# Performance work log

Measured on AMD Instinct MI355X. Metric: run time of the kernel, lower is better.

The kernel has to match this reference:

```python
import jax, jax.numpy as jnp
import numpy as np

EPS = 1e-6

def setup_inputs() -> dict:
    key = jax.random.key(0)
    kq, kk, kv = jax.random.split(key, 3)
    n, L, h, d = 4, 8192, 8, 64
    queries = jax.random.normal(kq, (n, L, h, d), dtype=jnp.float32)
    keys = jax.random.normal(kk, (n, L, h, d), dtype=jnp.float32)
    values = jax.random.normal(kv, (n, L, h, d), dtype=jnp.float32)
    return {"queries": queries, "keys": keys, "values": values}

def reference(queries, keys, values):
    d = queries.shape[-1]
    temp = d ** (-0.25)  # softmax_temp default e**-0.25
    # elu feature map: phi(x) = elu(x) + 1  (applied after temperature scaling)
    q = jax.nn.elu(queries * temp) + 1.0  # [n, l, h, d]
    k = jax.nn.elu(keys * temp) + 1.0     # [n, s, h, d]
    # associative kv state: [n, h, m, d]
    kv = jnp.einsum('nshd,nshm->nhmd', k, values)
    # normalizer z: [n, l, h]
    z = 1.0 / (jnp.einsum('nlhd,nhd->nlh', q, k.sum(axis=1)) + EPS)
    # output: [n, l, h, m]
    v = jnp.einsum('nlhd,nhmd,nlh->nlhm', q, kv, z)
    # module returns v.transpose(-3, -2) -> [n, h, l, m]
    return jnp.swapaxes(v, 1, 2)
```

## Files before the change

### kernel.cpp

```cpp
#include <hip/hip_runtime.h>
#include <hip/hip_bf16.h>

#define NN 4
#define LL 8192
#define HH 8
#define DD 64
#define NH 32
#define RS  (HH*DD)
#define KV_ELEMS 4160
#define CCH 32

typedef __attribute__((ext_vector_type(8))) short bf16x8;
typedef __attribute__((ext_vector_type(4))) float f32x4;

__device__ __forceinline__ float phi(float x) {
  float t = x * 0.35355339059327373f;
  return t > 0.f ? t + 1.f : __expf(t);
}
__device__ __forceinline__ short f2bf(float x) {
  __hip_bfloat16 h = __float2bfloat16(x);
  return (short)__builtin_bit_cast(unsigned short, h);
}
__device__ __forceinline__ float bf2f(short s) {
  __hip_bfloat16 h = __builtin_bit_cast(__hip_bfloat16, (unsigned short)s);
  return __bfloat162float(h);
}
__device__ __forceinline__ void split2(float x, short& hi, short& lo) {
  hi = f2bf(x);
  lo = f2bf(x - bf2f(hi));
}

__global__ __launch_bounds__(256) void kv_partial_kernel(
    const float* __restrict__ K, const float* __restrict__ V,
    float* __restrict__ part, int sch)
{
  const int nh    = blockIdx.x / sch;
  const int chunk = blockIdx.x % sch;
  const int n = nh >> 3, h = nh & 7;
  const int tid = threadIdx.x;
  const int w = tid >> 6, lane = tid & 63;
  const int q = lane >> 4, p = lane & 15;
  const int d_super = (w >> 1) * 32, m_super = (w & 1) * 32;
  const int rows_pb = LL / sch;
  const int s_base  = chunk * rows_pb;

  const float* kbase = K + ((size_t)n * LL * HH + h) * DD;
  const float* vbase = V + ((size_t)n * LL * HH + h) * DD;

  f32x4 acc[2][2] = {};
  float ksacc[2] = {0.f, 0.f};

  for (int step = 0; step < rows_pb / 32; ++step) {
    const int s0 = s_base + step * 32 + q * 8;

    bf16x8 ahi[2], alo[2];
#pragma unroll
    for (int dt = 0; dt < 2; ++dt) {
      const float* kp = kbase + (size_t)s0 * RS + d_super + dt * 16 + p;
      float f[8];
#pragma unroll
      for (int j = 0; j < 8; ++j) f[j] = phi(kp[(size_t)j * RS]);
#pragma unroll
      for (int j = 0; j < 8; ++j) ksacc[dt] += f[j];
#pragma unroll
      for (int j = 0; j < 8; ++j) { short hi, lo; split2(f[j], hi, lo); ahi[dt][j] = hi; alo[dt][j] = lo; }
    }

    bf16x8 bhi[2], blo[2];
#pragma unroll
    for (int mt = 0; mt < 2; ++mt) {
      const float* vp = vbase + (size_t)s0 * RS + m_super + mt * 16 + p;
      float f[8];
#pragma unroll
      for (int j = 0; j < 8; ++j) f[j] = vp[(size_t)j * RS];
#pragma unroll
      for (int j = 0; j < 8; ++j) { short hi, lo; split2(f[j], hi, lo); bhi[mt][j] = hi; blo[mt][j] = lo; }
    }

#pragma unroll
    for (int dt = 0; dt < 2; ++dt)
#pragma unroll
      for (int mt = 0; mt < 2; ++mt) {
        acc[dt][mt] = __builtin_amdgcn_mfma_f32_16x16x32_bf16(ahi[dt], bhi[mt], acc[dt][mt], 0, 0, 0);
        acc[dt][mt] = __builtin_amdgcn_mfma_f32_16x16x32_bf16(ahi[dt], blo[mt], acc[dt][mt], 0, 0, 0);
        acc[dt][mt] = __builtin_amdgcn_mfma_f32_16x16x32_bf16(alo[dt], bhi[mt], acc[dt][mt], 0, 0, 0);
      }
  }

#pragma unroll
  for (int dt = 0; dt < 2; ++dt) {
    ksacc[dt] += __shfl_xor(ksacc[dt], 16, 64);
    ksacc[dt] += __shfl_xor(ksacc[dt], 32, 64);
  }

  float* po = part + (size_t)blockIdx.x * KV_ELEMS;
#pragma unroll
  for (int dt = 0; dt < 2; ++dt)
#pragma unroll
    for (int mt = 0; mt < 2; ++mt) {
      const int row = d_super + dt * 16 + q * 4;
      const int col = m_super + mt * 16 + p;
#pragma unroll
      for (int r = 0; r < 4; ++r)
        po[(row + r) * 64 + col] = acc[dt][mt][r];
    }
  if ((w & 1) == 0 && q < 2)
    po[4096 + d_super + q * 16 + p] = ksacc[q];
}

__global__ __launch_bounds__(256) void kv_reduce_kernel(
    const float* __restrict__ part, short* __restrict__ kvh,
    short* __restrict__ kvl, float* __restrict__ ksum, int np)
{
  const int nh = blockIdx.x / 17;
  const int e  = (blockIdx.x % 17) * 256 + threadIdx.x;
  if (e >= KV_ELEMS) return;
  const float* pp = part + (size_t)nh * np * KV_ELEMS + e;
  float s = 0.f;
  for (int i = 0; i < np; ++i) s += pp[(size_t)i * KV_ELEMS];
  if (e < 4096) {
    const int d = e >> 6, m = e & 63;
    short hi, lo; split2(s, hi, lo);
    kvh[(size_t)nh * 4096 + m * 64 + d] = hi;
    kvl[(size_t)nh * 4096 + m * 64 + d] = lo;
  } else {
    ksum[(size_t)nh * 64 + (e - 4096)] = s;
  }
}

__global__ __launch_bounds__(256) void attn_out_kernel(
    const float* __restrict__ Q, const short* __restrict__ kvh,
    const short* __restrict__ kvl, const float* __restrict__ ksumg,
    float* __restrict__ out)
{
  const int nh    = blockIdx.x / CCH;
  const int chunk = blockIdx.x % CCH;
  const int n = nh >> 3, h = nh & 7;
  const int tid = threadIdx.x;
  const int w = tid >> 6, lane = tid & 63;
  const int q = lane >> 4, p = lane & 15;
  const int m_super = (w & 1) * 32;
  const int rows_pb = LL / CCH;
  const int row_base = chunk * rows_pb + (w >> 1) * (rows_pb / 2);

  const float* qbase = Q + ((size_t)n * LL * HH + h) * DD;

  bf16x8 bh[2][2], bl[2][2];
#pragma unroll
  for (int mt = 0; mt < 2; ++mt)
#pragma unroll
    for (int kst = 0; kst < 2; ++kst) {
      const size_t off = (size_t)nh * 4096 + (m_super + mt * 16 + p) * 64 + kst * 32 + q * 8;
      bh[mt][kst] = *(const bf16x8*)(kvh + off);
      bl[mt][kst] = *(const bf16x8*)(kvl + off);
    }
  float ksr[2][8];
#pragma unroll
  for (int kst = 0; kst < 2; ++kst) {
    const float* kp = ksumg + (size_t)nh * 64 + kst * 32 + q * 8;
    float4 a = *(const float4*)(kp), b = *(const float4*)(kp + 4);
    ksr[kst][0]=a.x; ksr[kst][1]=a.y; ksr[kst][2]=a.z; ksr[kst][3]=a.w;
    ksr[kst][4]=b.x; ksr[kst][5]=b.y; ksr[kst][6]=b.z; ksr[kst][7]=b.w;
  }

  for (int lt = 0; lt < rows_pb / 2 / 16; ++lt) {
    const int l0 = row_base + lt * 16;
    f32x4 acc[2] = {};
    float zpart = 0.f;

#pragma unroll
    for (int kst = 0; kst < 2; ++kst) {
      const float* qp = qbase + (size_t)(l0 + p) * RS + kst * 32 + q * 8;
      float4 f0 = *(const float4*)(qp), f1 = *(const float4*)(qp + 4);
      float f[8] = {f0.x, f0.y, f0.z, f0.w, f1.x, f1.y, f1.z, f1.w};
      bf16x8 ah, al;
#pragma unroll
      for (int j = 0; j < 8; ++j) {
        f[j] = phi(f[j]);
        short hi, lo; split2(f[j], hi, lo);
        ah[j] = hi; al[j] = lo;
        zpart += f[j] * ksr[kst][j];
      }
#pragma unroll
      for (int mt = 0; mt < 2; ++mt) {
        acc[mt] = __builtin_amdgcn_mfma_f32_16x16x32_bf16(ah, bh[mt][kst], acc[mt], 0, 0, 0);
        acc[mt] = __builtin_amdgcn_mfma_f32_16x16x32_bf16(ah, bl[mt][kst], acc[mt], 0, 0, 0);
        acc[mt] = __builtin_amdgcn_mfma_f32_16x16x32_bf16(al, bh[mt][kst], acc[mt], 0, 0, 0);
      }
    }

    zpart += __shfl_xor(zpart, 16, 64);
    zpart += __shfl_xor(zpart, 32, 64);
    const float z = 1.0f / (zpart + 1e-6f);
    float zr[4];
#pragma unroll
    for (int r = 0; r < 4; ++r) zr[r] = __shfl(z, q * 4 + r, 64);

#pragma unroll
    for (int mt = 0; mt < 2; ++mt) {
      const int col = m_super + mt * 16 + p;
#pragma unroll
      for (int r = 0; r < 4; ++r) {
        const int row = l0 + q * 4 + r;
        out[((size_t)nh * LL + row) * DD + col] = acc[mt][r] * zr[r];
      }
    }
  }
}

extern "C" void kernel_launch(void* const* d_in, const int* in_sizes, int n_in,
                              void* d_out, int out_size, void* d_ws, size_t ws_size,
                              hipStream_t stream)
{
  const float* Q = (const float*)d_in[0];
  const float* K = (const float*)d_in[1];
  const float* V = (const float*)d_in[2];
  float* out = (float*)d_out;

  int sch = 32;
  while (sch > 1) {
    size_t need = (size_t)NH * sch * KV_ELEMS * 4
                + (size_t)NH * 4096 * 2 * 2
                + (size_t)NH * 64 * 4;
    if (need <= ws_size) break;
    sch >>= 1;
  }
  float* part = (float*)d_ws;
  short* kvh  = (short*)((char*)d_ws + (size_t)NH * sch * KV_ELEMS * 4);
  short* kvl  = kvh + (size_t)NH * 4096;
  float* ksum = (float*)(kvl + (size_t)NH * 4096);

  hipLaunchKernelGGL(kv_partial_kernel, dim3(NH * sch), dim3(256), 0, stream,
                     K, V, part, sch);
  hipLaunchKernelGGL(kv_reduce_kernel, dim3(NH * 17), dim3(256), 0, stream,
                     part, kvh, kvl, ksum, sch);
  hipLaunchKernelGGL(attn_out_kernel, dim3(NH * CCH), dim3(256), 0, stream,
                     Q, kvh, kvl, ksum, out);
}
```

Baseline: 253.4 us.

## Stage K/V tiles through LDS with vectorized loads and register prefetch

Reworks the KV-partial kernel. Each thread now issues coalesced float4 loads of K and V rows and computes phi and the bf16 hi/lo split once per element. The split values are written transposed into LDS, and MFMA operands are read back from LDS. Before, the kernel did strided scalar global loads, and the four warps redundantly applied phi and split to overlapping K/V data. The next tile is prefetched into registers while MFMAs run, and the k-sum is reduced through LDS. This adds barriers and LDS traffic, and launch bounds now request 4 blocks per CU.

```diff
diff --git a/kernel.cpp b/kernel.cpp
--- a/kernel.cpp
+++ b/kernel.cpp
@@ -29,8 +29,12 @@
   hi = f2bf(x);
   lo = f2bf(x - bf2f(hi));
 }
-
-__global__ __launch_bounds__(256) void kv_partial_kernel(
+__device__ __forceinline__ int pk2(short a, short b) {
+  return (int)(((unsigned)(unsigned short)a) | (((unsigned)(unsigned short)b) << 16));
+}
+#define MFMA16 __builtin_amdgcn_mfma_f32_16x16x32_bf16
+
+__global__ __launch_bounds__(256, 4) void kv_partial_kernel(
     const float* __restrict__ K, const float* __restrict__ V,
     float* __restrict__ part, int sch)
 {
@@ -40,72 +44,102 @@
   const int tid = threadIdx.x;
   const int w = tid >> 6, lane = tid & 63;
   const int q = lane >> 4, p = lane & 15;
-  const int d_super = (w >> 1) * 32, m_super = (w & 1) * 32;
+  const int dsup = (w >> 1) * 32, msup = (w & 1) * 32;
+  const int g = tid >> 4, c = tid & 15;
   const int rows_pb = LL / sch;
+  const int ntiles  = rows_pb / 64;
   const int s_base  = chunk * rows_pb;
 
   const float* kbase = K + ((size_t)n * LL * HH + h) * DD;
   const float* vbase = V + ((size_t)n * LL * HH + h) * DD;
 
+  __shared__ __align__(16) short lds4[4][64][72];
+
   f32x4 acc[2][2] = {};
-  float ksacc[2] = {0.f, 0.f};
-
-  for (int step = 0; step < rows_pb / 32; ++step) {
-    const int s0 = s_base + step * 32 + q * 8;
-
-    bf16x8 ahi[2], alo[2];
-#pragma unroll
-    for (int dt = 0; dt < 2; ++dt) {
-      const float* kp = kbase + (size_t)s0 * RS + d_super + dt * 16 + p;
-      float f[8];
-#pragma unroll
-      for (int j = 0; j < 8; ++j) f[j] = phi(kp[(size_t)j * RS]);
-#pragma unroll
-      for (int j = 0; j < 8; ++j) ksacc[dt] += f[j];
-#pragma unroll
-      for (int j = 0; j < 8; ++j) { short hi, lo; split2(f[j], hi, lo); ahi[dt][j] = hi; alo[dt][j] = lo; }
-    }
-
-    bf16x8 bhi[2], blo[2];
+  float ksp[4] = {0.f, 0.f, 0.f, 0.f};
+  f32x4 kf[4], vf[4];
+
+#define LOADT(T) { \
+    const float* kp_ = kbase + (size_t)(s_base + (T) * 64 + 4 * g) * RS + 4 * c; \
+    const float* vp_ = vbase + (size_t)(s_base + (T) * 64 + 4 * g) * RS + 4 * c; \
+    kf[0] = *(const f32x4*)(kp_);          vf[0] = *(const f32x4*)(vp_); \
+    kf[1] = *(const f32x4*)(kp_ + RS);     vf[1] = *(const f32x4*)(vp_ + RS); \
+    kf[2] = *(const f32x4*)(kp_ + 2*RS);   vf[2] = *(const f32x4*)(vp_ + 2*RS); \
+    kf[3] = *(const f32x4*)(kp_ + 3*RS);   vf[3] = *(const f32x4*)(vp_ + 3*RS); }
+
+  LOADT(0);
+
+  for (int tile = 0; tile < ntiles; ++tile) {
+#pragma unroll
+    for (int j = 0; j < 4; ++j) {
+      short sh[4], sl[4];
+#pragma unroll
+      for (int u = 0; u < 4; ++u) {
+        float f = phi(kf[u][j]);
+        ksp[j] += f;
+        split2(f, sh[u], sl[u]);
+      }
+      *(int2*)&lds4[0][4*c + j][4*g] = make_int2(pk2(sh[0], sh[1]), pk2(sh[2], sh[3]));
+      *(int2*)&lds4[1][4*c + j][4*g] = make_int2(pk2(sl[0], sl[1]), pk2(sl[2], sl[3]));
+#pragma unroll
+      for (int u = 0; u < 4; ++u) split2(vf[u][j], sh[u], sl[u]);
+      *(int2*)&lds4[2][4*c + j][4*g] = make_int2(pk2(sh[0], sh[1]), pk2(sh[2], sh[3]));
+      *(int2*)&lds4[3][4*c + j][4*g] = make_int2(pk2(sl[0], sl[1]), pk2(sl[2], sl[3]));
+    }
+    __syncthreads();
+
+    if (tile + 1 < ntiles) LOADT(tile + 1);
+
+#pragma unroll
+    for (int ks = 0; ks < 2; ++ks) {
+      const int so = ks * 32 + q * 8;
+      bf16x8 ah[2], al[2], bh[2], bl[2];
+#pragma unroll
+      for (int dt = 0; dt < 2; ++dt) {
+        ah[dt] = *(const bf16x8*)&lds4[0][dsup + dt * 16 + p][so];
+        al[dt] = *(const bf16x8*)&lds4[1][dsup + dt * 16 + p][so];
+      }
+#pragma unroll
+      for (int mt = 0; mt < 2; ++mt) {
+        bh[mt] = *(const bf16x8*)&lds4[2][msup + mt * 16 + p][so];
+        bl[mt] = *(const bf16x8*)&lds4[3][msup + mt * 16 + p][so];
+      }
+#pragma unroll
+      for (int dt = 0; dt < 2; ++dt)
+#pragma unroll
+        for (int mt = 0; mt < 2; ++mt) {
+          acc[dt][mt] = MFMA16(ah[dt], bh[mt], acc[dt][mt], 0, 0, 0);
+          acc[dt][mt] = MFMA16(ah[dt], bl[mt], acc[dt][mt], 0, 0, 0);
+          acc[dt][mt] = MFMA16(al[dt], bh[mt], acc[dt][mt], 0, 0, 0);
+        }
+    }
+    __syncthreads();
+  }
+#undef LOADT
+
+  float* po = part + (size_t)blockIdx.x * KV_ELEMS;
+#pragma unroll
+  for (int dt = 0; dt < 2; ++dt)
 #pragma unroll
     for (int mt = 0; mt < 2; ++mt) {
-      const float* vp = vbase + (size_t)s0 * RS + m_super + mt * 16 + p;
-      float f[8];
-#pragma unroll
-      for (int j = 0; j < 8; ++j) f[j] = vp[(size_t)j * RS];
-#pragma unroll
-      for (int j = 0; j < 8; ++j) { short hi, lo; split2(f[j], hi, lo); bhi[mt][j] = hi; blo[mt][j] = lo; }
-    }
-
-#pragma unroll
-    for (int dt = 0; dt < 2; ++dt)
-#pragma unroll
-      for (int mt = 0; mt < 2; ++mt) {
-        acc[dt][mt] = __builtin_amdgcn_mfma_f32_16x16x32_bf16(ahi[dt], bhi[mt], acc[dt][mt], 0, 0, 0);
-        acc[dt][mt] = __builtin_amdgcn_mfma_f32_16x16x32_bf16(ahi[dt], blo[mt], acc[dt][mt], 0, 0, 0);
-        acc[dt][mt] = __builtin_amdgcn_mfma_f32_16x16x32_bf16(alo[dt], bhi[mt], acc[dt][mt], 0, 0, 0);
-      }
-  }
-
-#pragma unroll
-  for (int dt = 0; dt < 2; ++dt) {
-    ksacc[dt] += __shfl_xor(ksacc[dt], 16, 64);
-    ksacc[dt] += __shfl_xor(ksacc[dt], 32, 64);
-  }
-
-  float* po = part + (size_t)blockIdx.x * KV_ELEMS;
-#pragma unroll
-  for (int dt = 0; dt < 2; ++dt)
-#pragma unroll
-    for (int mt = 0; mt < 2; ++mt) {
-      const int row = d_super + dt * 16 + q * 4;
-      const int col = m_super + mt * 16 + p;
+      const int row = dsup + dt * 16 + q * 4;
+      const int col = msup + mt * 16 + p;
 #pragma unroll
       for (int r = 0; r < 4; ++r)
         po[(row + r) * 64 + col] = acc[dt][mt][r];
     }
-  if ((w & 1) == 0 && q < 2)
-    po[4096 + d_super + q * 16 + p] = ksacc[q];
+
+  float* ksl = (float*)lds4;
+  f32x4 kq = {ksp[0], ksp[1], ksp[2], ksp[3]};
+  *(f32x4*)&ksl[tid * 4] = kq;
+  __syncthreads();
+  if (tid < 64) {
+    float s = 0.f;
+#pragma unroll
+    for (int gg = 0; gg < 16; ++gg)
+      s += ksl[(gg * 16 + (tid >> 2)) * 4 + (tid & 3)];
+    po[4096 + tid] = s;
+  }
 }
 
 __global__ __launch_bounds__(256) void kv_reduce_kernel(
@@ -183,9 +217,9 @@
       }
 #pragma unroll
       for (int mt = 0; mt < 2; ++mt) {
-        acc[mt] = __builtin_amdgcn_mfma_f32_16x16x32_bf16(ah, bh[mt][kst], acc[mt], 0, 0, 0);
-        acc[mt] = __builtin_amdgcn_mfma_f32_16x16x32_bf16(ah, bl[mt][kst], acc[mt], 0, 0, 0);
-        acc[mt] = __builtin_amdgcn_mfma_f32_16x16x32_bf16(al, bh[mt][kst], acc[mt], 0, 0, 0);
+        acc[mt] = MFMA16(ah, bh[mt][kst], acc[mt], 0, 0, 0);
+        acc[mt] = MFMA16(ah, bl[mt][kst], acc[mt], 0, 0, 0);
+        acc[mt] = MFMA16(al, bh[mt][kst], acc[mt], 0, 0, 0);
       }
     }
 
```

Measured after the change: 258.2 us. About the same (+1.9%).

## Restructure KV and output kernels to load all heads per row coalesced via LDS

Applied to the files above, without the earlier changes.

Both main kernels now assign one block per batch and row chunk, with 512 threads covering all 8 heads. Each block loads full contiguous rows of K/V/Q with vectorized reads, stages them in shared memory and prefetches the next tile into registers. This replaces the previous strided per-head gathers, which touched only 64 floats of each 512-float row. The KV partial product switches from bf16-split MFMA to FP32 FMA register tiles. The output kernel now has each wave handle one head with all 64 output columns. The partial-buffer layout and the reduce indexing change to match. In exchange there are more LDS barriers, heavier register use per thread, and scalar FMA in place of matrix-core throughput for the KV product.

```diff
diff --git a/kernel.cpp b/kernel.cpp
--- a/kernel.cpp
+++ b/kernel.cpp
@@ -8,7 +8,7 @@
 #define NH 32
 #define RS  (HH*DD)
 #define KV_ELEMS 4160
-#define CCH 32
+#define CCH 64
 
 typedef __attribute__((ext_vector_type(8))) short bf16x8;
 typedef __attribute__((ext_vector_type(4))) float f32x4;
@@ -29,83 +29,95 @@
   hi = f2bf(x);
   lo = f2bf(x - bf2f(hi));
 }
-
-__global__ __launch_bounds__(256) void kv_partial_kernel(
+#define MFMA16 __builtin_amdgcn_mfma_f32_16x16x32_bf16
+
+__global__ __launch_bounds__(512, 2) void kv_partial_kernel(
     const float* __restrict__ K, const float* __restrict__ V,
     float* __restrict__ part, int sch)
 {
-  const int nh    = blockIdx.x / sch;
-  const int chunk = blockIdx.x % sch;
-  const int n = nh >> 3, h = nh & 7;
+  const int n = blockIdx.x / sch, chunk = blockIdx.x % sch;
   const int tid = threadIdx.x;
-  const int w = tid >> 6, lane = tid & 63;
-  const int q = lane >> 4, p = lane & 15;
-  const int d_super = (w >> 1) * 32, m_super = (w & 1) * 32;
+  const int h  = tid >> 6;
+  const int t6 = tid & 63;
+  const int d0 = ((t6 >> 3) & 7) * 8;
+  const int m0 = (t6 & 7) * 8;
+  const int hc = h * 64;
+  const int sr = tid >> 6, sc = (tid & 63) * 8;
   const int rows_pb = LL / sch;
-  const int s_base  = chunk * rows_pb;
-
-  const float* kbase = K + ((size_t)n * LL * HH + h) * DD;
-  const float* vbase = V + ((size_t)n * LL * HH + h) * DD;
-
-  f32x4 acc[2][2] = {};
-  float ksacc[2] = {0.f, 0.f};
-
-  for (int step = 0; step < rows_pb / 32; ++step) {
-    const int s0 = s_base + step * 32 + q * 8;
-
-    bf16x8 ahi[2], alo[2];
-#pragma unroll
-    for (int dt = 0; dt < 2; ++dt) {
-      const float* kp = kbase + (size_t)s0 * RS + d_super + dt * 16 + p;
-      float f[8];
-#pragma unroll
-      for (int j = 0; j < 8; ++j) f[j] = phi(kp[(size_t)j * RS]);
-#pragma unroll
-      for (int j = 0; j < 8; ++j) ksacc[dt] += f[j];
-#pragma unroll
-      for (int j = 0; j < 8; ++j) { short hi, lo; split2(f[j], hi, lo); ahi[dt][j] = hi; alo[dt][j] = lo; }
-    }
-
-    bf16x8 bhi[2], blo[2];
-#pragma unroll
-    for (int mt = 0; mt < 2; ++mt) {
-      const float* vp = vbase + (size_t)s0 * RS + m_super + mt * 16 + p;
-      float f[8];
-#pragma unroll
-      for (int j = 0; j < 8; ++j) f[j] = vp[(size_t)j * RS];
-#pragma unroll
-      for (int j = 0; j < 8; ++j) { short hi, lo; split2(f[j], hi, lo); bhi[mt][j] = hi; blo[mt][j] = lo; }
-    }
-
-#pragma unroll
-    for (int dt = 0; dt < 2; ++dt)
-#pragma unroll
-      for (int mt = 0; mt < 2; ++mt) {
-        acc[dt][mt] = __builtin_amdgcn_mfma_f32_16x16x32_bf16(ahi[dt], bhi[mt], acc[dt][mt], 0, 0, 0);
-        acc[dt][mt] = __builtin_amdgcn_mfma_f32_16x16x32_bf16(ahi[dt], blo[mt], acc[dt][mt], 0, 0, 0);
-        acc[dt][mt] = __builtin_amdgcn_mfma_f32_16x16x32_bf16(alo[dt], bhi[mt], acc[dt][mt], 0, 0, 0);
-      }
-  }
-
-#pragma unroll
-  for (int dt = 0; dt < 2; ++dt) {
-    ksacc[dt] += __shfl_xor(ksacc[dt], 16, 64);
-    ksacc[dt] += __shfl_xor(ksacc[dt], 32, 64);
-  }
-
-  float* po = part + (size_t)blockIdx.x * KV_ELEMS;
-#pragma unroll
-  for (int dt = 0; dt < 2; ++dt)
-#pragma unroll
-    for (int mt = 0; mt < 2; ++mt) {
-      const int row = d_super + dt * 16 + q * 4;
-      const int col = m_super + mt * 16 + p;
-#pragma unroll
-      for (int r = 0; r < 4; ++r)
-        po[(row + r) * 64 + col] = acc[dt][mt][r];
-    }
-  if ((w & 1) == 0 && q < 2)
-    po[4096 + d_super + q * 16 + p] = ksacc[q];
+  const int nt = rows_pb / 8;
+
+  const float* kbase = K + ((size_t)n * LL + (size_t)chunk * rows_pb) * RS;
+  const float* vbase = V + ((size_t)n * LL + (size_t)chunk * rows_pb) * RS;
+
+  __shared__ float kls[8][520];
+  __shared__ float vls[8][520];
+
+  float acc[8][8] = {};
+  float ksacc[8] = {};
+  f32x4 kr[2], vr[2];
+
+  auto loada = [&](int T) {
+    const float* kp_ = kbase + ((size_t)T * 8 + sr) * RS + sc;
+    const float* vp_ = vbase + ((size_t)T * 8 + sr) * RS + sc;
+    kr[0] = *(const f32x4*)(kp_);     kr[1] = *(const f32x4*)(kp_ + 4);
+    vr[0] = *(const f32x4*)(vp_);     vr[1] = *(const f32x4*)(vp_ + 4);
+  };
+
+  loada(0);
+  for (int t = 0; t < nt; ++t) {
+    f32x4 kw0, kw1;
+#pragma unroll
+    for (int jj = 0; jj < 4; ++jj) {
+      float f0 = phi(kr[0][jj]);
+      float f1 = phi(kr[1][jj]);
+      ksacc[jj]     += f0;
+      ksacc[jj + 4] += f1;
+      kw0[jj] = f0; kw1[jj] = f1;
+    }
+    *(f32x4*)&kls[sr][sc]     = kw0;
+    *(f32x4*)&kls[sr][sc + 4] = kw1;
+    *(f32x4*)&vls[sr][sc]     = vr[0];
+    *(f32x4*)&vls[sr][sc + 4] = vr[1];
+    __syncthreads();
+    if (t + 1 < nt) loada(t + 1);
+
+#pragma unroll 2
+    for (int s = 0; s < 8; ++s) {
+      const f32x4 k0 = *(const f32x4*)&kls[s][hc + d0];
+      const f32x4 k1 = *(const f32x4*)&kls[s][hc + d0 + 4];
+      const f32x4 v0 = *(const f32x4*)&vls[s][hc + m0];
+      const f32x4 v1 = *(const f32x4*)&vls[s][hc + m0 + 4];
+#pragma unroll
+      for (int i = 0; i < 4; ++i)
+#pragma unroll
+        for (int j = 0; j < 4; ++j) {
+          acc[i][j]         = fmaf(k0[i], v0[j], acc[i][j]);
+          acc[i][j + 4]     = fmaf(k0[i], v1[j], acc[i][j + 4]);
+          acc[i + 4][j]     = fmaf(k1[i], v0[j], acc[i + 4][j]);
+          acc[i + 4][j + 4] = fmaf(k1[i], v1[j], acc[i + 4][j + 4]);
+        }
+    }
+    __syncthreads();
+  }
+
+  float* po = part + ((size_t)blockIdx.x * 8 + h) * KV_ELEMS;
+#pragma unroll
+  for (int i = 0; i < 8; ++i) {
+    f32x4 o0 = {acc[i][0], acc[i][1], acc[i][2], acc[i][3]};
+    f32x4 o1 = {acc[i][4], acc[i][5], acc[i][6], acc[i][7]};
+    *(f32x4*)&po[(d0 + i) * 64 + m0]     = o0;
+    *(f32x4*)&po[(d0 + i) * 64 + m0 + 4] = o1;
+  }
+
+#pragma unroll
+  for (int j = 0; j < 8; ++j) vls[sr][sc + j] = ksacc[j];
+  __syncthreads();
+  {
+    float s = 0.f;
+#pragma unroll
+    for (int r = 0; r < 8; ++r) s += vls[r][tid];
+    part[((size_t)blockIdx.x * 8 + (tid >> 6)) * KV_ELEMS + 4096 + (tid & 63)] = s;
+  }
 }
 
 __global__ __launch_bounds__(256) void kv_reduce_kernel(
@@ -115,9 +127,10 @@
   const int nh = blockIdx.x / 17;
   const int e  = (blockIdx.x % 17) * 256 + threadIdx.x;
   if (e >= KV_ELEMS) return;
-  const float* pp = part + (size_t)nh * np * KV_ELEMS + e;
+  const int n = nh >> 3, hh = nh & 7;
+  const float* pp = part + ((size_t)(n * np) * 8 + hh) * KV_ELEMS + e;
   float s = 0.f;
-  for (int i = 0; i < np; ++i) s += pp[(size_t)i * KV_ELEMS];
+  for (int i = 0; i < np; ++i) s += pp[(size_t)i * 8 * KV_ELEMS];
   if (e < 4096) {
     const int d = e >> 6, m = e & 63;
     short hi, lo; split2(s, hi, lo);
@@ -128,29 +141,32 @@
   }
 }
 
-__global__ __launch_bounds__(256) void attn_out_kernel(
+__global__ __launch_bounds__(512, 2) void attn_out_kernel(
     const float* __restrict__ Q, const short* __restrict__ kvh,
     const short* __restrict__ kvl, const float* __restrict__ ksumg,
     float* __restrict__ out)
 {
-  const int nh    = blockIdx.x / CCH;
-  const int chunk = blockIdx.x % CCH;
-  const int n = nh >> 3, h = nh & 7;
+  const int n = blockIdx.x / CCH, chunk = blockIdx.x % CCH;
   const int tid = threadIdx.x;
   const int w = tid >> 6, lane = tid & 63;
   const int q = lane >> 4, p = lane & 15;
-  const int m_super = (w & 1) * 32;
+  const int nh = n * 8 + w;
   const int rows_pb = LL / CCH;
-  const int row_base = chunk * rows_pb + (w >> 1) * (rows_pb / 2);
-
-  const float* qbase = Q + ((size_t)n * LL * HH + h) * DD;
-
-  bf16x8 bh[2][2], bl[2][2];
-#pragma unroll
-  for (int mt = 0; mt < 2; ++mt)
+  const int nt = rows_pb / 16;
+  const int l_base = chunk * rows_pb;
+  const int sr = tid >> 5, sc = (tid & 31) * 16;
+
+  const float* qbase = Q + (size_t)n * LL * RS;
+
+  __shared__ short qh[16][520];
+  __shared__ short ql[16][520];
+
+  bf16x8 bh[4][2], bl[4][2];
+#pragma unroll
+  for (int mt = 0; mt < 4; ++mt)
 #pragma unroll
     for (int kst = 0; kst < 2; ++kst) {
-      const size_t off = (size_t)nh * 4096 + (m_super + mt * 16 + p) * 64 + kst * 32 + q * 8;
+      const size_t off = (size_t)nh * 4096 + (size_t)(mt * 16 + p) * 64 + kst * 32 + q * 8;
       bh[mt][kst] = *(const bf16x8*)(kvh + off);
       bl[mt][kst] = *(const bf16x8*)(kvl + off);
     }
@@ -158,53 +174,82 @@
 #pragma unroll
   for (int kst = 0; kst < 2; ++kst) {
     const float* kp = ksumg + (size_t)nh * 64 + kst * 32 + q * 8;
-    float4 a = *(const float4*)(kp), b = *(const float4*)(kp + 4);
-    ksr[kst][0]=a.x; ksr[kst][1]=a.y; ksr[kst][2]=a.z; ksr[kst][3]=a.w;
-    ksr[kst][4]=b.x; ksr[kst][5]=b.y; ksr[kst][6]=b.z; ksr[kst][7]=b.w;
-  }
-
-  for (int lt = 0; lt < rows_pb / 2 / 16; ++lt) {
-    const int l0 = row_base + lt * 16;
-    f32x4 acc[2] = {};
-    float zpart = 0.f;
-
+    f32x4 a = *(const f32x4*)(kp), b = *(const f32x4*)(kp + 4);
+    ksr[kst][0]=a[0]; ksr[kst][1]=a[1]; ksr[kst][2]=a[2]; ksr[kst][3]=a[3];
+    ksr[kst][4]=b[0]; ksr[kst][5]=b[1]; ksr[kst][6]=b[2]; ksr[kst][7]=b[3];
+  }
+
+  f32x4 qa[4], qb[4];
+  auto loadq = [&](f32x4* R, int T) {
+    const float* qp_ = qbase + (size_t)(l_base + T * 16 + sr) * RS + sc;
+    R[0] = *(const f32x4*)(qp_);      R[1] = *(const f32x4*)(qp_ + 4);
+    R[2] = *(const f32x4*)(qp_ + 8);  R[3] = *(const f32x4*)(qp_ + 12);
+  };
+
+  auto cbody = [&](const f32x4* R, int T) {
+    bf16x8 hv0, hv1, lv0, lv1;
+#pragma unroll
+    for (int r = 0; r < 2; ++r)
+#pragma unroll
+      for (int jj = 0; jj < 4; ++jj) {
+        float f = phi(R[r][jj]);
+        short hs, ls; split2(f, hs, ls);
+        hv0[r * 4 + jj] = hs; lv0[r * 4 + jj] = ls;
+      }
+#pragma unroll
+    for (int r = 0; r < 2; ++r)
+#pragma unroll
+      for (int jj = 0; jj < 4; ++jj) {
+        float f = phi(R[r + 2][jj]);
+        short hs, ls; split2(f, hs, ls);
+        hv1[r * 4 + jj] = hs; lv1[r * 4 + jj] = ls;
+      }
+    *(bf16x8*)&qh[sr][sc]     = hv0;  *(bf16x8*)&qh[sr][sc + 8] = hv1;
+    *(bf16x8*)&ql[sr][sc]     = lv0;  *(bf16x8*)&ql[sr][sc + 8] = lv1;
+    __syncthreads();
+
+    f32x4 acc[4] = {};
+    float zp = 0.f;
+    bf16x8 ah[2], al[2];
 #pragma unroll
     for (int kst = 0; kst < 2; ++kst) {
-      const float* qp = qbase + (size_t)(l0 + p) * RS + kst * 32 + q * 8;
-      float4 f0 = *(const float4*)(qp), f1 = *(const float4*)(qp + 4);
-      float f[8] = {f0.x, f0.y, f0.z, f0.w, f1.x, f1.y, f1.z, f1.w};
-      bf16x8 ah, al;
-#pragma unroll
-      for (int j = 0; j < 8; ++j) {
-        f[j] = phi(f[j]);
-        short hi, lo; split2(f[j], hi, lo);
-        ah[j] = hi; al[j] = lo;
-        zpart += f[j] * ksr[kst][j];
+      const int cc = w * 64 + kst * 32 + q * 8;
+      ah[kst] = *(const bf16x8*)&qh[p][cc];
+      al[kst] = *(const bf16x8*)&ql[p][cc];
+#pragma unroll
+      for (int j = 0; j < 8; ++j)
+        zp += (bf2f(ah[kst][j]) + bf2f(al[kst][j])) * ksr[kst][j];
+    }
+#pragma unroll
+    for (int kst = 0; kst < 2; ++kst)
+#pragma unroll
+      for (int mt = 0; mt < 4; ++mt) {
+        acc[mt] = MFMA16(ah[kst], bh[mt][kst], acc[mt], 0, 0, 0);
+        acc[mt] = MFMA16(ah[kst], bl[mt][kst], acc[mt], 0, 0, 0);
+        acc[mt] = MFMA16(al[kst], bh[mt][kst], acc[mt], 0, 0, 0);
       }
-#pragma unroll
-      for (int mt = 0; mt < 2; ++mt) {
-        acc[mt] = __builtin_amdgcn_mfma_f32_16x16x32_bf16(ah, bh[mt][kst], acc[mt], 0, 0, 0);
-        acc[mt] = __builtin_amdgcn_mfma_f32_16x16x32_bf16(ah, bl[mt][kst], acc[mt], 0, 0, 0);
-        acc[mt] = __builtin_amdgcn_mfma_f32_16x16x32_bf16(al, bh[mt][kst], acc[mt], 0, 0, 0);
-      }
-    }
-
-    zpart += __shfl_xor(zpart, 16, 64);
-    zpart += __shfl_xor(zpart, 32, 64);
-    const float z = 1.0f / (zpart + 1e-6f);
+    zp += __shfl_xor(zp, 16, 64);
+    zp += __shfl_xor(zp, 32, 64);
+    const float z = 1.0f / (zp + 1e-6f);
     float zr[4];
 #pragma unroll
     for (int r = 0; r < 4; ++r) zr[r] = __shfl(z, q * 4 + r, 64);
 
-#pragma unroll
-    for (int mt = 0; mt < 2; ++mt) {
-      const int col = m_super + mt * 16 + p;
-#pragma unroll
-      for (int r = 0; r < 4; ++r) {
-        const int row = l0 + q * 4 + r;
-        out[((size_t)nh * LL + row) * DD + col] = acc[mt][r] * zr[r];
-      }
-    }
+    const int l0 = l_base + T * 16;
+#pragma unroll
+    for (int mt = 0; mt < 4; ++mt)
+#pragma unroll
+      for (int r = 0; r < 4; ++r)
+        out[((size_t)nh * LL + l0 + q * 4 + r) * DD + mt * 16 + p] = acc[mt][r] * zr[r];
+    __syncthreads();
+  };
+
+  loadq(qa, 0);
+  for (int t = 0; t < nt; t += 2) {
+    loadq(qb, t + 1);
+    cbody(qa, t);
+    if (t + 2 < nt) loadq(qa, t + 2);
+    cbody(qb, t + 1);
   }
 }
 
@@ -217,23 +262,23 @@
   const float* V = (const float*)d_in[2];
   float* out = (float*)d_out;
 
-  int sch = 32;
-  while (sch > 1) {
-    size_t need = (size_t)NH * sch * KV_ELEMS * 4
+  int sch = 64;
+  while (sch > 4) {
+    size_t need = (size_t)NN * sch * 8 * KV_ELEMS * 4
                 + (size_t)NH * 4096 * 2 * 2
                 + (size_t)NH * 64 * 4;
     if (need <= ws_size) break;
     sch >>= 1;
   }
   float* part = (float*)d_ws;
-  short* kvh  = (short*)((char*)d_ws + (size_t)NH * sch * KV_ELEMS * 4);
+  short* kvh  = (short*)((char*)d_ws + (size_t)NN * sch * 8 * KV_ELEMS * 4);
   short* kvl  = kvh + (size_t)NH * 4096;
   float* ksum = (float*)(kvl + (size_t)NH * 4096);
 
-  hipLaunchKernelGGL(kv_partial_kernel, dim3(NH * sch), dim3(256), 0, stream,
+  hipLaunchKernelGGL(kv_partial_kernel, dim3(NN * sch), dim3(512), 0, stream,
                      K, V, part, sch);
   hipLaunchKernelGGL(kv_reduce_kernel, dim3(NH * 17), dim3(256), 0, stream,
                      part, kvh, kvl, ksum, sch);
-  hipLaunchKernelGGL(attn_out_kernel, dim3(NH * CCH), dim3(256), 0, stream,
+  hipLaunchKernelGGL(attn_out_kernel, dim3(NN * CCH), dim3(512), 0, stream,
                      Q, kvh, kvl, ksum, out);
 }
```

Result: faster. 241.4 us (-4.7%).
